# Kernel optimization log

Measured on AMD Instinct MI355X. Metric: run time of the kernel, lower is better.

The kernel has to match this reference:

```python
import jax, jax.numpy as jnp
import numpy as np

N, E, G = 16384, 131072, 32
EPS = 1e-5


def seg_sum(x, ids, n):
    return jax.ops.segment_sum(x, ids, num_segments=n)


def seg_max(x, ids, n):
    return jax.ops.segment_max(x, ids, num_segments=n)


def gcn_conv(x, w, b, src, dst, n):
    # PyG GCNConv: add self loops, symmetric deg normalization
    loop = jnp.arange(n)
    s = jnp.concatenate([src, loop])
    d = jnp.concatenate([dst, loop])
    deg = seg_sum(jnp.ones_like(d, dtype=x.dtype), d, n)
    dis = jax.lax.rsqrt(deg)
    h = x @ w
    norm = (dis[s] * dis[d])[:, None]
    return seg_sum(h[s] * norm, d, n) + b


def sage_conv(x, wl, wr, b, src, dst, n):
    # mean aggregation of source features into target nodes
    cnt = seg_sum(jnp.ones_like(dst, dtype=x.dtype), dst, n)
    agg = seg_sum(x[src], dst, n) / jnp.maximum(cnt, 1.0)[:, None]
    return agg @ wl + x @ wr + b


def gat_conv(x, w, a_src, a_dst, b, src, dst, n, heads=4, ch=256):
    loop = jnp.arange(n)
    s = jnp.concatenate([src, loop])
    d = jnp.concatenate([dst, loop])
    h = (x @ w).reshape(n, heads, ch)            # [N,H,C]
    es = jnp.sum(h * a_src, axis=-1)             # [N,H]
    ed = jnp.sum(h * a_dst, axis=-1)             # [N,H]
    e = jax.nn.leaky_relu(es[s] + ed[d], 0.2)    # [E2,H]
    m = seg_max(e, d, n)
    ex = jnp.exp(e - m[d])
    z = seg_sum(ex, d, n)
    alpha = ex / z[d]                            # softmax over incoming edges
    out = seg_sum(h[s] * alpha[:, :, None], d, n)  # [N,H,C]
    return out.mean(axis=1) + b                  # concat=False -> head mean


def batchnorm(x, g, b):
    mu = x.mean(axis=0)
    var = x.var(axis=0)
    return (x - mu) * jax.lax.rsqrt(var + EPS) * g + b


def setup_inputs() -> dict:
    key = jax.random.key(0)
    ks = jax.random.split(key, 16)
    def w(k, shape, fan_in):
        return jax.random.normal(k, shape, jnp.float32) * (1.0 / np.sqrt(fan_in))
    return {
        "x": jax.random.uniform(ks[0], (N, 5), jnp.float32),
        "edge_index": jax.random.randint(ks[1], (2, E), 0, N),
        "batch": jnp.sort(jax.random.randint(ks[2], (N,), 0, G)),
        "gcn1_w": w(ks[3], (5, 64), 5), "gcn1_b": jnp.zeros((64,), jnp.float32),
        "sage_wl": w(ks[4], (64, 128), 64), "sage_wr": w(ks[5], (64, 128), 64),
        "sage_b": jnp.zeros((128,), jnp.float32),
        "gat_w": w(ks[6], (128, 1024), 128),
        "gat_asrc": w(ks[7], (4, 256), 256), "gat_adst": w(ks[8], (4, 256), 256),
        "gat_b": jnp.zeros((256,), jnp.float32),
        "gcn4_w": w(ks[9], (256, 512), 256), "gcn4_b": jnp.zeros((512,), jnp.float32),
        "bn1_g": jnp.ones((64,), jnp.float32), "bn1_b": jnp.zeros((64,), jnp.float32),
        "bn2_g": jnp.ones((128,), jnp.float32), "bn2_b": jnp.zeros((128,), jnp.float32),
        "bn3_g": jnp.ones((256,), jnp.float32), "bn3_b": jnp.zeros((256,), jnp.float32),
        "bn4_g": jnp.ones((512,), jnp.float32), "bn4_b": jnp.zeros((512,), jnp.float32),
        "fc_w": w(ks[10], (1024, 1024), 1024), "fc_b": jnp.zeros((1024,), jnp.float32),
    }


def reference(x, edge_index, batch, gcn1_w, gcn1_b, sage_wl, sage_wr, sage_b,
              gat_w, gat_asrc, gat_adst, gat_b, gcn4_w, gcn4_b,
              bn1_g, bn1_b, bn2_g, bn2_b, bn3_g, bn3_b, bn4_g, bn4_b,
              fc_w, fc_b):
    src, dst = edge_index[0], edge_index[1]
    n = x.shape[0]
    h = jax.nn.relu(batchnorm(gcn_conv(x, gcn1_w, gcn1_b, src, dst, n), bn1_g, bn1_b))
    h = jax.nn.relu(batchnorm(sage_conv(h, sage_wl, sage_wr, sage_b, src, dst, n), bn2_g, bn2_b))
    h = jax.nn.relu(batchnorm(gat_conv(h, gat_w, gat_asrc, gat_adst, gat_b, src, dst, n), bn3_g, bn3_b))
    h = jax.nn.relu(batchnorm(gcn_conv(h, gcn4_w, gcn4_b, src, dst, n), bn4_g, bn4_b))
    # global mean / max pooling over graphs in the batch
    cnt = seg_sum(jnp.ones((n,), h.dtype), batch, G)
    mean_p = seg_sum(h, batch, G) / jnp.maximum(cnt, 1.0)[:, None]
    max_p = seg_max(h, batch, G)
    max_p = jnp.where(cnt[:, None] > 0, max_p, 0.0)
    pooled = jnp.concatenate([mean_p, max_p], axis=1)  # [G,1024]
    return pooled @ fc_w + fc_b
```

## Files before the change

### kernel.cpp

```cpp
#include <hip/hip_runtime.h>

#define N_ 16384
#define E_ 131072
#define G_ 32
#define EPSF 1e-5f

typedef unsigned short bf16u;
typedef __attribute__((ext_vector_type(8))) short s8v;
typedef __attribute__((ext_vector_type(4))) float f4v;

__device__ __forceinline__ bf16u f2bf(float v) {
    union { float f; unsigned u; } x; x.f = v;
    unsigned r = x.u + 0x7FFF + ((x.u >> 16) & 1);
    return (bf16u)(r >> 16);
}
__device__ __forceinline__ float bf2f(bf16u u) {
    union { unsigned u; float f; } x; x.u = (unsigned)u << 16;
    return x.f;
}

static const size_t OFF_INDEG = 0;
static const size_t OFF_ROWS  = 65536;
static const size_t OFF_CURSOR= 131584;
static const size_t OFF_CSR   = 197120;
static const size_t OFF_DIS   = 721408;
static const size_t OFF_ES    = 786944;
static const size_t OFF_ED    = 1049088;
static const size_t OFF_BNS   = 1311232;
static const size_t OFF_BNQ   = 1376768;
static const size_t OFF_GB    = 1442304;
static const size_t OFF_CNT   = 1442444;
static const size_t OFF_POOL  = 1442560;
static const size_t OFF_MSET  = 1573632;
static const size_t OFF_PART  = 1573632;
static const size_t OFF_BN1C  = 1578752;
static const size_t OFF_XA    = 1786624;
static const size_t OFF_AB    = 5980928;
static const size_t OFF_H2P   = 10175232;
static const size_t OFF_H2B   = 14369536;
static const size_t OFF_H3B   = 18563840;
static const size_t OFF_AGG   = 35328768;
static const size_t OFF_XA4B  = 52105984;
static const size_t OFF_WT1   = 68883200;
static const size_t OFF_WT2   = 69145344;
static const size_t OFF_WT3   = 69407488;
static const size_t OFF_H4B   = 69440256;
static const size_t OFF_VES   = 86479616;
static const size_t OFF_VED   = 86481664;

__global__ __launch_bounds__(1024) void k_scan(const int* __restrict__ indeg,
                                               int* __restrict__ rows,
                                               int* __restrict__ cursor,
                                               float* __restrict__ dis) {
    __shared__ int part[1024];
    int t = threadIdx.x;
    int base = t * 16;
    int local[16];
    int s = 0;
#pragma unroll
    for (int i = 0; i < 16; ++i) {
        local[i] = indeg[base + i]; s += local[i];
        dis[base + i] = rsqrtf((float)local[i] + 1.0f);
    }
    part[t] = s;
    __syncthreads();
    for (int off = 1; off < 1024; off <<= 1) {
        int v = (t >= off) ? part[t - off] : 0;
        __syncthreads();
        part[t] += v;
        __syncthreads();
    }
    int run = (t == 0) ? 0 : part[t - 1];
#pragma unroll
    for (int i = 0; i < 16; ++i) {
        rows[base + i] = run; cursor[base + i] = run; run += local[i];
    }
    if (t == 1023) rows[N_] = run;
}

__global__ void k_fill(const int* __restrict__ src, const int* __restrict__ dst,
                       int* __restrict__ cursor, int* __restrict__ csr) {
    int e = blockIdx.x * 256 + threadIdx.x;
    if (e < E_) {
        int p = atomicAdd(&cursor[dst[e]], 1);
        csr[p] = src[e];
    }
}

__global__ void k_wconv_all(const float* __restrict__ gat_w,
                            const float* __restrict__ gcn4_w,
                            const float* __restrict__ wl, const float* __restrict__ wr,
                            const int* __restrict__ batch,
                            const float* __restrict__ gat_as,
                            const float* __restrict__ gat_ad,
                            const int* __restrict__ dstE,
                            bf16u* __restrict__ wT1, bf16u* __restrict__ wT2,
                            bf16u* __restrict__ wT3, int* __restrict__ gb,
                            float* __restrict__ ves, float* __restrict__ ved,
                            int* __restrict__ indeg) {
    int idx = blockIdx.x * 256 + threadIdx.x;
    if (idx < 131072) {
        int c = idx >> 9;
        int kk = idx & 511;
        int h = kk >> 7, k = kk & 127;
        wT1[idx] = f2bf(0.25f * gat_w[(size_t)k * 1024 + h * 256 + c]);
    } else if (idx < 262144) {
        int j = idx - 131072;
        int m = j >> 8, k = j & 255;
        wT2[j] = f2bf(gcn4_w[(size_t)k * 512 + m]);
    } else if (idx < 278528) {
        int j = idx - 262144;
        int m = j >> 7, k = j & 127;
        float v = (k < 64) ? wl[k*128 + m] : wr[(k-64)*128 + m];
        wT3[j] = f2bf(v);
    } else if (idx < 278592) {
        int g = idx - 278528;
        if (g > G_) return;
        if (g == G_) { gb[G_] = N_; return; }
        int lo = 0, hi = N_;
        while (lo < hi) { int mid = (lo + hi) >> 1; if (batch[mid] < g) lo = mid + 1; else hi = mid; }
        gb[g] = lo;
    } else if (idx < 279104) {
        int j = idx - 278592;
        int h = j >> 7, k = j & 127;
        float s = 0.f;
        for (int c = 0; c < 256; ++c)
            s += gat_w[(size_t)k * 1024 + h*256 + c] * gat_as[h*256 + c];
        ves[j] = s;
    } else if (idx < 279616) {
        int j = idx - 279104;
        int h = j >> 7, k = j & 127;
        float s = 0.f;
        for (int c = 0; c < 256; ++c)
            s += gat_w[(size_t)k * 1024 + h*256 + c] * gat_ad[h*256 + c];
        ved[j] = s;
    } else if (idx < 410688) {
        int e = idx - 279616;
        atomicAdd(&indeg[dstE[e]], 1);
    }
}

__global__ __launch_bounds__(256) void k_gcn1x(const float* __restrict__ x,
                                               const float* __restrict__ dis,
                                               const int* __restrict__ rows,
                                               const int* __restrict__ csr,
                                               float* __restrict__ xa) {
    int wave = threadIdx.x >> 6, lane = threadIdx.x & 63;
    int i = blockIdx.x * 4 + wave;
    float a0=0,a1=0,a2=0,a3=0,a4=0;
    int e0 = rows[i], e1 = rows[i+1];
    for (int e = e0 + lane; e < e1; e += 64) {
        int s = csr[e];
        float wt = dis[s];
        a0 += x[s*5+0]*wt; a1 += x[s*5+1]*wt; a2 += x[s*5+2]*wt;
        a3 += x[s*5+3]*wt; a4 += x[s*5+4]*wt;
    }
#pragma unroll
    for (int off = 32; off > 0; off >>= 1) {
        a0 += __shfl_xor(a0, off, 64); a1 += __shfl_xor(a1, off, 64);
        a2 += __shfl_xor(a2, off, 64); a3 += __shfl_xor(a3, off, 64);
        a4 += __shfl_xor(a4, off, 64);
    }
    float di = dis[i];
    float v0 = di*(a0 + di*x[i*5+0]);
    float v1 = di*(a1 + di*x[i*5+1]);
    float v2 = di*(a2 + di*x[i*5+2]);
    float v3 = di*(a3 + di*x[i*5+3]);
    float v4 = di*(a4 + di*x[i*5+4]);
    if (lane < 5) {
        float v = lane == 0 ? v0 : lane == 1 ? v1 : lane == 2 ? v2 : lane == 3 ? v3 : v4;
        xa[(size_t)i*8 + lane] = v;
    }
}

__global__ __launch_bounds__(256) void k_xstats(const float* __restrict__ xa,
                                                float* __restrict__ partial,
                                                int* __restrict__ cnt,
                                                const float* __restrict__ w,
                                                const float* __restrict__ b,
                                                const float* __restrict__ bng,
                                                const float* __restrict__ bnb,
                                                float* __restrict__ sc,
                                                float* __restrict__ sh) {
    __shared__ float wsum[80];
    __shared__ int lastFlag;
    int t = threadIdx.x;
    int tid = blockIdx.x * 256 + t;
    float v0 = xa[(size_t)tid*8+0], v1 = xa[(size_t)tid*8+1], v2 = xa[(size_t)tid*8+2];
    float v3 = xa[(size_t)tid*8+3], v4 = xa[(size_t)tid*8+4];
    float m[20];
    m[0]=v0; m[1]=v1; m[2]=v2; m[3]=v3; m[4]=v4;
    m[5]=v0*v0;  m[6]=v0*v1;  m[7]=v0*v2;  m[8]=v0*v3;  m[9]=v0*v4;
    m[10]=v1*v1; m[11]=v1*v2; m[12]=v1*v3; m[13]=v1*v4;
    m[14]=v2*v2; m[15]=v2*v3; m[16]=v2*v4;
    m[17]=v3*v3; m[18]=v3*v4;
    m[19]=v4*v4;
#pragma unroll
    for (int off = 32; off > 0; off >>= 1)
#pragma unroll
        for (int j = 0; j < 20; ++j) m[j] += __shfl_xor(m[j], off, 64);
    int wave = t >> 6, lane = t & 63;
    if (lane == 0)
#pragma unroll
        for (int j = 0; j < 20; ++j) wsum[wave*20 + j] = m[j];
    __syncthreads();
    if (t < 20) {
        partial[blockIdx.x * 20 + t] = wsum[t] + wsum[20+t] + wsum[40+t] + wsum[60+t];
        __threadfence();
    }
    __syncthreads();
    if (t == 0) lastFlag = (atomicAdd(cnt, 1) == 63);
    __syncthreads();
    if (!lastFlag || t >= 64) return;
    int l = t;
    const float invN = 1.0f / (float)N_;
    float mm[20];
#pragma unroll
    for (int j = 0; j < 20; ++j) {
        float v = partial[l*20 + j];
#pragma unroll
        for (int off = 32; off > 0; off >>= 1) v += __shfl_xor(v, off, 64);
        mm[j] = v * invN;
    }
    int c = l;
    float wc0 = w[c], wc1 = w[64+c], wc2 = w[128+c], wc3 = w[192+c], wc4 = w[256+c];
    float mu = b[c] + mm[0]*wc0 + mm[1]*wc1 + mm[2]*wc2 + mm[3]*wc3 + mm[4]*wc4;
    float var = 0.f;
    var += (mm[5]  - mm[0]*mm[0]) * wc0*wc0;
    var += (mm[6]  - mm[0]*mm[1]) * wc0*wc1 * 2.f;
    var += (mm[7]  - mm[0]*mm[2]) * wc0*wc2 * 2.f;
    var += (mm[8]  - mm[0]*mm[3]) * wc0*wc3 * 2.f;
    var += (mm[9]  - mm[0]*mm[4]) * wc0*wc4 * 2.f;
    var += (mm[10] - mm[1]*mm[1]) * wc1*wc1;
    var += (mm[11] - mm[1]*mm[2]) * wc1*wc2 * 2.f;
    var += (mm[12] - mm[1]*mm[3]) * wc1*wc3 * 2.f;
    var += (mm[13] - mm[1]*mm[4]) * wc1*wc4 * 2.f;
    var += (mm[14] - mm[2]*mm[2]) * wc2*wc2;
    var += (mm[15] - mm[2]*mm[3]) * wc2*wc3 * 2.f;
    var += (mm[16] - mm[2]*mm[4]) * wc2*wc4 * 2.f;
    var += (mm[17] - mm[3]*mm[3]) * wc3*wc3;
    var += (mm[18] - mm[3]*mm[4]) * wc3*wc4 * 2.f;
    var += (mm[19] - mm[4]*mm[4]) * wc4*wc4;
    float scale = rsqrtf(var + EPSF) * bng[c];
    sc[c] = scale;
    sh[c] = fmaf(b[c], scale, bnb[c] - mu * scale);
}

__global__ __launch_bounds__(256) void k_sage_l1(const float* __restrict__ xa,
                                                 const float* __restrict__ sc,
                                                 const float* __restrict__ sh,
                                                 const float* __restrict__ w,
                                                 const int* __restrict__ rows,
                                                 const int* __restrict__ csr,
                                                 bf16u* __restrict__ ab) {
    int wave = threadIdx.x >> 6, lane = threadIdx.x & 63;
    int i = blockIdx.x * 4 + wave;
    int c = lane;
    float wc0 = w[c], wc1 = w[64+c], wc2 = w[128+c], wc3 = w[192+c], wc4 = w[256+c];
    float scale = sc[c], base = sh[c];
    {
        float4 p = *(const float4*)&xa[(size_t)i*8];
        float p4 = xa[(size_t)i*8 + 4];
        float t = p.x*wc0 + p.y*wc1 + p.z*wc2 + p.w*wc3 + p4*wc4;
        float v = fmaf(t, scale, base); v = v > 0.f ? v : 0.f;
        ab[(size_t)i*128 + 64 + c] = f2bf(v);
    }
    int e0 = rows[i], e1 = rows[i+1];
    float s = 0.f;
    int e = e0;
    for (; e + 3 < e1; e += 4) {
        int s0 = csr[e], s1 = csr[e+1], s2 = csr[e+2], s3 = csr[e+3];
        float4 q0 = *(const float4*)&xa[(size_t)s0*8]; float r0 = xa[(size_t)s0*8+4];
        float4 q1 = *(const float4*)&xa[(size_t)s1*8]; float r1 = xa[(size_t)s1*8+4];
        float4 q2 = *(const float4*)&xa[(size_t)s2*8]; float r2 = xa[(size_t)s2*8+4];
        float4 q3 = *(const float4*)&xa[(size_t)s3*8]; float r3 = xa[(size_t)s3*8+4];
        float t0 = q0.x*wc0 + q0.y*wc1 + q0.z*wc2 + q0.w*wc3 + r0*wc4;
        float t1 = q1.x*wc0 + q1.y*wc1 + q1.z*wc2 + q1.w*wc3 + r1*wc4;
        float t2 = q2.x*wc0 + q2.y*wc1 + q2.z*wc2 + q2.w*wc3 + r2*wc4;
        float t3 = q3.x*wc0 + q3.y*wc1 + q3.z*wc2 + q3.w*wc3 + r3*wc4;
        float v;
        v = fmaf(t0, scale, base); s += v > 0.f ? v : 0.f;
        v = fmaf(t1, scale, base); s += v > 0.f ? v : 0.f;
        v = fmaf(t2, scale, base); s += v > 0.f ? v : 0.f;
        v = fmaf(t3, scale, base); s += v > 0.f ? v : 0.f;
    }
    for (; e < e1; ++e) {
        int sI = csr[e];
        float4 q = *(const float4*)&xa[(size_t)sI*8]; float r = xa[(size_t)sI*8+4];
        float t = q.x*wc0 + q.y*wc1 + q.z*wc2 + q.w*wc3 + r*wc4;
        float v = fmaf(t, scale, base); s += v > 0.f ? v : 0.f;
    }
    ab[(size_t)i*128 + c] = f2bf(s / fmaxf((float)(e1 - e0), 1.0f));
}

__global__ __launch_bounds__(256) void k_gemm_mfma(const bf16u* __restrict__ A,
                                                   const bf16u* __restrict__ BT,
                                                   const float* __restrict__ bias,
                                                   bf16u* __restrict__ C,
                                                   float* __restrict__ sum,
                                                   float* __restrict__ sumsq,
                                                   int K, int M) {
    __shared__ bf16u As[128][40];
    __shared__ bf16u Bs[128][40];
    int tid = threadIdx.x;
    int wave = tid >> 6, lane = tid & 63;
    int wr = (wave >> 1) * 64, wc = (wave & 1) * 64;
    int row0 = blockIdx.y * 128, col0 = blockIdx.x * 128;
    f4v acc[4][4];
#pragma unroll
    for (int i = 0; i < 4; ++i)
#pragma unroll
        for (int j = 0; j < 4; ++j) acc[i][j] = (f4v)0.0f;

    int sr = tid >> 1;
    int sh = (tid & 1) * 16;
    int lr = lane & 15, lq = lane >> 4;

    for (int k0 = 0; k0 < K; k0 += 32) {
        const bf16u* ap = A + (size_t)(row0 + sr) * K + k0 + sh;
        *(uint4*)&As[sr][sh]     = *(const uint4*)ap;
        *(uint4*)&As[sr][sh + 8] = *(const uint4*)(ap + 8);
        const bf16u* bp = BT + (size_t)(col0 + sr) * K + k0 + sh;
        *(uint4*)&Bs[sr][sh]     = *(const uint4*)bp;
        *(uint4*)&Bs[sr][sh + 8] = *(const uint4*)(bp + 8);
        __syncthreads();
        s8v af[4], bfr[4];
#pragma unroll
        for (int i = 0; i < 4; ++i)
            af[i] = *(const s8v*)&As[wr + i*16 + lr][lq*8];
#pragma unroll
        for (int j = 0; j < 4; ++j)
            bfr[j] = *(const s8v*)&Bs[wc + j*16 + lr][lq*8];
#pragma unroll
        for (int i = 0; i < 4; ++i)
#pragma unroll
            for (int j = 0; j < 4; ++j)
                acc[i][j] = __builtin_amdgcn_mfma_f32_16x16x32_bf16(af[i], bfr[j], acc[i][j], 0, 0, 0);
        __syncthreads();
    }

    int slot = (blockIdx.y & 7) << 9;
#pragma unroll
    for (int j = 0; j < 4; ++j) {
        int col = col0 + wc + j*16 + lr;
        float bv = bias ? bias[col] : 0.f;
        float s = 0.f, q = 0.f;
#pragma unroll
        for (int i = 0; i < 4; ++i) {
#pragma unroll
            for (int r = 0; r < 4; ++r) {
                float v = acc[i][j][r] + bv;
                int row = row0 + wr + i*16 + lq*4 + r;
                C[(size_t)row * M + col] = f2bf(v);
                s += v; q += v*v;
            }
        }
        if (sum) {
            s += __shfl_xor(s, 16, 64); q += __shfl_xor(q, 16, 64);
            s += __shfl_xor(s, 32, 64); q += __shfl_xor(q, 32, 64);
            if (lq == 0) { atomicAdd(&sum[slot + col], s); atomicAdd(&sumsq[slot + col], q); }
        }
    }
}

__global__ __launch_bounds__(256) void k_bn_apply2b_attn(
        const bf16u* __restrict__ hp, const float* __restrict__ sum,
        const float* __restrict__ sumsq, const float* __restrict__ g,
        const float* __restrict__ b, const float* __restrict__ ves,
        const float* __restrict__ ved, bf16u* __restrict__ hb,
        float* __restrict__ es, float* __restrict__ ed) {
    int wave = threadIdx.x >> 6, lane = threadIdx.x & 63;
    int i = blockIdx.x * 4 + wave;
    int c = lane * 2;
    const float invN = 1.0f / (float)N_;
    float sx=0.f, sy=0.f, qx=0.f, qy=0.f;
#pragma unroll
    for (int s8 = 0; s8 < 8; ++s8) {
        float2 a = *(const float2*)&sum[s8*512 + c];
        float2 d = *(const float2*)&sumsq[s8*512 + c];
        sx += a.x; sy += a.y; qx += d.x; qy += d.y;
    }
    float2 gg = *(const float2*)&g[c];
    float2 bb = *(const float2*)&b[c];
    float mu0 = sx*invN, mu1 = sy*invN;
    float sc0 = rsqrtf(qx*invN - mu0*mu0 + EPSF)*gg.x, sh0 = bb.x - mu0*sc0;
    float sc1 = rsqrtf(qy*invN - mu1*mu1 + EPSF)*gg.y, sh1 = bb.y - mu1*sc1;
    unsigned pv = *(const unsigned*)&hp[(size_t)i*128 + c];
    float v0 = bf2f((bf16u)(pv & 0xFFFF));
    float v1 = bf2f((bf16u)(pv >> 16));
    v0 = fmaf(v0, sc0, sh0); v0 = v0 > 0.f ? v0 : 0.f;
    v1 = fmaf(v1, sc1, sh1); v1 = v1 > 0.f ? v1 : 0.f;
    unsigned ow = (unsigned)f2bf(v0) | ((unsigned)f2bf(v1) << 16);
    *(unsigned*)&hb[(size_t)i*128 + c] = ow;
    float vs[4], vd[4];
#pragma unroll
    for (int h = 0; h < 4; ++h) {
        float2 a = *(const float2*)&ves[h*128 + c];
        float2 d = *(const float2*)&ved[h*128 + c];
        vs[h] = v0*a.x + v1*a.y;
        vd[h] = v0*d.x + v1*d.y;
    }
#pragma unroll
    for (int off = 32; off > 0; off >>= 1) {
#pragma unroll
        for (int h = 0; h < 4; ++h) {
            vs[h] += __shfl_xor(vs[h], off, 64);
            vd[h] += __shfl_xor(vd[h], off, 64);
        }
    }
    if (lane == 0) {
        *(float4*)&es[i*4] = make_float4(vs[0], vs[1], vs[2], vs[3]);
        *(float4*)&ed[i*4] = make_float4(vd[0], vd[1], vd[2], vd[3]);
    }
}

__global__ __launch_bounds__(256) void k_gat_agg2(const bf16u* __restrict__ h2b,
                                                  const float* __restrict__ es,
                                                  const float* __restrict__ ed,
                                                  const int* __restrict__ rows,
                                                  const int* __restrict__ csr,
                                                  bf16u* __restrict__ agg) {
    int wave = threadIdx.x >> 6, lane = threadIdx.x & 63;
    int i = blockIdx.x * 4 + wave;
    int c = lane * 2;
    float4 edv = *(const float4*)&ed[i*4];
    float4 sv  = *(const float4*)&es[i*4];
    int e0 = rows[i], e1 = rows[i+1];
    float e, m0, m1, m2, m3;
    e = sv.x + edv.x; m0 = e >= 0.f ? e : 0.2f*e;
    e = sv.y + edv.y; m1 = e >= 0.f ? e : 0.2f*e;
    e = sv.z + edv.z; m2 = e >= 0.f ? e : 0.2f*e;
    e = sv.w + edv.w; m3 = e >= 0.f ? e : 0.2f*e;
    for (int ee = e0 + lane; ee < e1; ee += 64) {
        int s = csr[ee];
        float4 s2 = *(const float4*)&es[s*4];
        e = s2.x + edv.x; m0 = fmaxf(m0, e >= 0.f ? e : 0.2f*e);
        e = s2.y + edv.y; m1 = fmaxf(m1, e >= 0.f ? e : 0.2f*e);
        e = s2.z + edv.z; m2 = fmaxf(m2, e >= 0.f ? e : 0.2f*e);
        e = s2.w + edv.w; m3 = fmaxf(m3, e >= 0.f ? e : 0.2f*e);
    }
#pragma unroll
    for (int off = 32; off > 0; off >>= 1) {
        m0 = fmaxf(m0, __shfl_xor(m0, off, 64));
        m1 = fmaxf(m1, __shfl_xor(m1, off, 64));
        m2 = fmaxf(m2, __shfl_xor(m2, off, 64));
        m3 = fmaxf(m3, __shfl_xor(m3, off, 64));
    }
    float z0, z1, z2, z3;
    float a00, a01, a10, a11, a20, a21, a30, a31;
    {
        e = sv.x + edv.x; e = e >= 0.f ? e : 0.2f*e; z0 = __expf(e - m0);
        e = sv.y + edv.y; e = e >= 0.f ? e : 0.2f*e; z1 = __expf(e - m1);
        e = sv.z + edv.z; e = e >= 0.f ? e : 0.2f*e; z2 = __expf(e - m2);
        e = sv.w + edv.w; e = e >= 0.f ? e : 0.2f*e; z3 = __expf(e - m3);
        unsigned pv = *(const unsigned*)&h2b[(size_t)i*128 + c];
        float v0 = bf2f((bf16u)(pv & 0xFFFF)), v1 = bf2f((bf16u)(pv >> 16));
        a00 = z0*v0; a01 = z0*v1; a10 = z1*v0; a11 = z1*v1;
        a20 = z2*v0; a21 = z2*v1; a30 = z3*v0; a31 = z3*v1;
    }
    int ee = e0;
    for (; ee + 3 < e1; ee += 4) {
        int s0 = csr[ee], s1 = csr[ee+1], s2i = csr[ee+2], s3i = csr[ee+3];
        float4 q0 = *(const float4*)&es[s0*4];
        float4 q1 = *(const float4*)&es[s1*4];
        float4 q2 = *(const float4*)&es[s2i*4];
        float4 q3 = *(const float4*)&es[s3i*4];
        unsigned p0 = *(const unsigned*)&h2b[(size_t)s0*128 + c];
        unsigned p1 = *(const unsigned*)&h2b[(size_t)s1*128 + c];
        unsigned p2 = *(const unsigned*)&h2b[(size_t)s2i*128 + c];
        unsigned p3 = *(const unsigned*)&h2b[(size_t)s3i*128 + c];
        float v0, v1, ex;
        v0 = bf2f((bf16u)(p0 & 0xFFFF)); v1 = bf2f((bf16u)(p0 >> 16));
        e = q0.x + edv.x; e = e >= 0.f ? e : 0.2f*e; ex = __expf(e - m0);
        z0 += ex; a00 = fmaf(ex, v0, a00); a01 = fmaf(ex, v1, a01);
        e = q0.y + edv.y; e = e >= 0.f ? e : 0.2f*e; ex = __expf(e - m1);
        z1 += ex; a10 = fmaf(ex, v0, a10); a11 = fmaf(ex, v1, a11);
        e = q0.z + edv.z; e = e >= 0.f ? e : 0.2f*e; ex = __expf(e - m2);
        z2 += ex; a20 = fmaf(ex, v0, a20); a21 = fmaf(ex, v1, a21);
        e = q0.w + edv.w; e = e >= 0.f ? e : 0.2f*e; ex = __expf(e - m3);
        z3 += ex; a30 = fmaf(ex, v0, a30); a31 = fmaf(ex, v1, a31);
        v0 = bf2f((bf16u)(p1 & 0xFFFF)); v1 = bf2f((bf16u)(p1 >> 16));
        e = q1.x + edv.x; e = e >= 0.f ? e : 0.2f*e; ex = __expf(e - m0);
        z0 += ex; a00 = fmaf(ex, v0, a00); a01 = fmaf(ex, v1, a01);
        e = q1.y + edv.y; e = e >= 0.f ? e : 0.2f*e; ex = __expf(e - m1);
        z1 += ex; a10 = fmaf(ex, v0, a10); a11 = fmaf(ex, v1, a11);
        e = q1.z + edv.z; e = e >= 0.f ? e : 0.2f*e; ex = __expf(e - m2);
        z2 += ex; a20 = fmaf(ex, v0, a20); a21 = fmaf(ex, v1, a21);
        e = q1.w + edv.w; e = e >= 0.f ? e : 0.2f*e; ex = __expf(e - m3);
        z3 += ex; a30 = fmaf(ex, v0, a30); a31 = fmaf(ex, v1, a31);
        v0 = bf2f((bf16u)(p2 & 0xFFFF)); v1 = bf2f((bf16u)(p2 >> 16));
        e = q2.x + edv.x; e = e >= 0.f ? e : 0.2f*e; ex = __expf(e - m0);
        z0 += ex; a00 = fmaf(ex, v0, a00); a01 = fmaf(ex, v1, a01);
        e = q2.y + edv.y; e = e >= 0.f ? e : 0.2f*e; ex = __expf(e - m1);
        z1 += ex; a10 = fmaf(ex, v0, a10); a11 = fmaf(ex, v1, a11);
        e = q2.z + edv.z; e = e >= 0.f ? e : 0.2f*e; ex = __expf(e - m2);
        z2 += ex; a20 = fmaf(ex, v0, a20); a21 = fmaf(ex, v1, a21);
        e = q2.w + edv.w; e = e >= 0.f ? e : 0.2f*e; ex = __expf(e - m3);
        z3 += ex; a30 = fmaf(ex, v0, a30); a31 = fmaf(ex, v1, a31);
        v0 = bf2f((bf16u)(p3 & 0xFFFF)); v1 = bf2f((bf16u)(p3 >> 16));
        e = q3.x + edv.x; e = e >= 0.f ? e : 0.2f*e; ex = __expf(e - m0);
        z0 += ex; a00 = fmaf(ex, v0, a00); a01 = fmaf(ex, v1, a01);
        e = q3.y + edv.y; e = e >= 0.f ? e : 0.2f*e; ex = __expf(e - m1);
        z1 += ex; a10 = fmaf(ex, v0, a10); a11 = fmaf(ex, v1, a11);
        e = q3.z + edv.z; e = e >= 0.f ? e : 0.2f*e; ex = __expf(e - m2);
        z2 += ex; a20 = fmaf(ex, v0, a20); a21 = fmaf(ex, v1, a21);
        e = q3.w + edv.w; e = e >= 0.f ? e : 0.2f*e; ex = __expf(e - m3);
        z3 += ex; a30 = fmaf(ex, v0, a30); a31 = fmaf(ex, v1, a31);
    }
    for (; ee < e1; ++ee) {
        int s = csr[ee];
        float4 s2 = *(const float4*)&es[s*4];
        unsigned pv = *(const unsigned*)&h2b[(size_t)s*128 + c];
        float v0 = bf2f((bf16u)(pv & 0xFFFF)), v1 = bf2f((bf16u)(pv >> 16));
        float ex;
        e = s2.x + edv.x; e = e >= 0.f ? e : 0.2f*e; ex = __expf(e - m0);
        z0 += ex; a00 = fmaf(ex, v0, a00); a01 = fmaf(ex, v1, a01);
        e = s2.y + edv.y; e = e >= 0.f ? e : 0.2f*e; ex = __expf(e - m1);
        z1 += ex; a10 = fmaf(ex, v0, a10); a11 = fmaf(ex, v1, a11);
        e = s2.z + edv.z; e = e >= 0.f ? e : 0.2f*e; ex = __expf(e - m2);
        z2 += ex; a20 = fmaf(ex, v0, a20); a21 = fmaf(ex, v1, a21);
        e = s2.w + edv.w; e = e >= 0.f ? e : 0.2f*e; ex = __expf(e - m3);
        z3 += ex; a30 = fmaf(ex, v0, a30); a31 = fmaf(ex, v1, a31);
    }
    size_t base = (size_t)i * 512 + c;
    float r; unsigned ow;
    r = 1.f/z0; ow = (unsigned)f2bf(a00*r) | ((unsigned)f2bf(a01*r) << 16);
    *(unsigned*)&agg[base]       = ow;
    r = 1.f/z1; ow = (unsigned)f2bf(a10*r) | ((unsigned)f2bf(a11*r) << 16);
    *(unsigned*)&agg[base + 128] = ow;
    r = 1.f/z2; ow = (unsigned)f2bf(a20*r) | ((unsigned)f2bf(a21*r) << 16);
    *(unsigned*)&agg[base + 256] = ow;
    r = 1.f/z3; ow = (unsigned)f2bf(a30*r) | ((unsigned)f2bf(a31*r) << 16);
    *(unsigned*)&agg[base + 384] = ow;
}

__global__ __launch_bounds__(256) void k_gcn4_agg(const bf16u* __restrict__ h3b,
                                                  const float* __restrict__ dis,
                                                  const int* __restrict__ rows,
                                                  const int* __restrict__ csr,
                                                  const float* __restrict__ sum,
                                                  const float* __restrict__ sumsq,
                                                  const float* __restrict__ g,
                                                  const float* __restrict__ b,
                                                  bf16u* __restrict__ xab) {
    int wave = threadIdx.x >> 6, q = threadIdx.x & 63;
    int i = blockIdx.x * 4 + wave;
    int c = q * 4;
    const float invN = 1.0f / (float)N_;
    float4 sm = make_float4(0.f,0.f,0.f,0.f), sq = make_float4(0.f,0.f,0.f,0.f);
#pragma unroll
    for (int s8 = 0; s8 < 8; ++s8) {
        float4 a = *(const float4*)&sum[s8*512 + c];
        float4 d = *(const float4*)&sumsq[s8*512 + c];
        sm.x += a.x; sm.y += a.y; sm.z += a.z; sm.w += a.w;
        sq.x += d.x; sq.y += d.y; sq.z += d.z; sq.w += d.w;
    }
    float4 gg = *(const float4*)&g[c];
    float4 bb = *(const float4*)&b[c];
    float mu, sc0, sc1, sc2, sc3, sh0, sh1, sh2, sh3;
    mu = sm.x*invN; sc0 = rsqrtf(sq.x*invN - mu*mu + EPSF)*gg.x; sh0 = bb.x - mu*sc0;
    mu = sm.y*invN; sc1 = rsqrtf(sq.y*invN - mu*mu + EPSF)*gg.y; sh1 = bb.y - mu*sc1;
    mu = sm.z*invN; sc2 = rsqrtf(sq.z*invN - mu*mu + EPSF)*gg.z; sh2 = bb.z - mu*sc2;
    mu = sm.w*invN; sc3 = rsqrtf(sq.w*invN - mu*mu + EPSF)*gg.w; sh3 = bb.w - mu*sc3;
    float di = dis[i];
    float a0, a1, a2, a3;
    {
        ushort4 u = *(const ushort4*)(h3b + (size_t)i*256 + c);
        float v, dd = di * di;
        v = fmaf(bf2f(u.x), sc0, sh0); v = v > 0.f ? v : 0.f; a0 = v * dd;
        v = fmaf(bf2f(u.y), sc1, sh1); v = v > 0.f ? v : 0.f; a1 = v * dd;
        v = fmaf(bf2f(u.z), sc2, sh2); v = v > 0.f ? v : 0.f; a2 = v * dd;
        v = fmaf(bf2f(u.w), sc3, sh3); v = v > 0.f ? v : 0.f; a3 = v * dd;
    }
    int e0 = rows[i], e1 = rows[i+1];
    int e = e0;
    for (; e + 3 < e1; e += 4) {
        int s0 = csr[e], s1 = csr[e+1], s2i = csr[e+2], s3i = csr[e+3];
        float w0 = dis[s0] * di, w1 = dis[s1] * di, w2 = dis[s2i] * di, w3 = dis[s3i] * di;
        ushort4 u0 = *(const ushort4*)(h3b + (size_t)s0*256 + c);
        ushort4 u1 = *(const ushort4*)(h3b + (size_t)s1*256 + c);
        ushort4 u2 = *(const ushort4*)(h3b + (size_t)s2i*256 + c);
        ushort4 u3 = *(const ushort4*)(h3b + (size_t)s3i*256 + c);
        float v;
        v = fmaf(bf2f(u0.x), sc0, sh0); v = v > 0.f ? v : 0.f; a0 += v * w0;
        v = fmaf(bf2f(u0.y), sc1, sh1); v = v > 0.f ? v : 0.f; a1 += v * w0;
        v = fmaf(bf2f(u0.z), sc2, sh2); v = v > 0.f ? v : 0.f; a2 += v * w0;
        v = fmaf(bf2f(u0.w), sc3, sh3); v = v > 0.f ? v : 0.f; a3 += v * w0;
        v = fmaf(bf2f(u1.x), sc0, sh0); v = v > 0.f ? v : 0.f; a0 += v * w1;
        v = fmaf(bf2f(u1.y), sc1, sh1); v = v > 0.f ? v : 0.f; a1 += v * w1;
        v = fmaf(bf2f(u1.z), sc2, sh2); v = v > 0.f ? v : 0.f; a2 += v * w1;
        v = fmaf(bf2f(u1.w), sc3, sh3); v = v > 0.f ? v : 0.f; a3 += v * w1;
        v = fmaf(bf2f(u2.x), sc0, sh0); v = v > 0.f ? v : 0.f; a0 += v * w2;
        v = fmaf(bf2f(u2.y), sc1, sh1); v = v > 0.f ? v : 0.f; a1 += v * w2;
        v = fmaf(bf2f(u2.z), sc2, sh2); v = v > 0.f ? v : 0.f; a2 += v * w2;
        v = fmaf(bf2f(u2.w), sc3, sh3); v = v > 0.f ? v : 0.f; a3 += v * w2;
        v = fmaf(bf2f(u3.x), sc0, sh0); v = v > 0.f ? v : 0.f; a0 += v * w3;
        v = fmaf(bf2f(u3.y), sc1, sh1); v = v > 0.f ? v : 0.f; a1 += v * w3;
        v = fmaf(bf2f(u3.z), sc2, sh2); v = v > 0.f ? v : 0.f; a2 += v * w3;
        v = fmaf(bf2f(u3.w), sc3, sh3); v = v > 0.f ? v : 0.f; a3 += v * w3;
    }
    for (; e < e1; ++e) {
        int s = csr[e];
        float w = dis[s] * di;
        ushort4 u = *(const ushort4*)(h3b + (size_t)s*256 + c);
        float v;
        v = fmaf(bf2f(u.x), sc0, sh0); v = v > 0.f ? v : 0.f; a0 += v * w;
        v = fmaf(bf2f(u.y), sc1, sh1); v = v > 0.f ? v : 0.f; a1 += v * w;
        v = fmaf(bf2f(u.z), sc2, sh2); v = v > 0.f ? v : 0.f; a2 += v * w;
        v = fmaf(bf2f(u.w), sc3, sh3); v = v > 0.f ? v : 0.f; a3 += v * w;
    }
    ushort4 o;
    o.x = f2bf(a0); o.y = f2bf(a1); o.z = f2bf(a2); o.w = f2bf(a3);
    *(ushort4*)(xab + (size_t)i*256 + c) = o;
}

__global__ void k_pool(const bf16u* __restrict__ h4b, const int* __restrict__ gb,
                       const float* __restrict__ sum, const float* __restrict__ sumsq,
                       const float* __restrict__ g, const float* __restrict__ b,
                       const float* __restrict__ fcb,
                       float* __restrict__ pooled, float* __restrict__ out) {
    int bidx = blockIdx.x;
    int t = threadIdx.x;
    if (bidx >= 512) {
        int i = (bidx - 512) * 256 + t;
        out[i] = fcb[i & 1023];
        return;
    }
    int gi = bidx >> 4;
    int chunk = bidx & 15;
    const float invN = 1.0f / (float)N_;
    float su0=0.f, qq0=0.f, su1=0.f, qq1=0.f;
#pragma unroll
    for (int s8 = 0; s8 < 8; ++s8) {
        su0 += sum[s8*512 + t];       qq0 += sumsq[s8*512 + t];
        su1 += sum[s8*512 + 256 + t]; qq1 += sumsq[s8*512 + 256 + t];
    }
    float mu0 = su0 * invN;
    float sc0 = rsqrtf(qq0 * invN - mu0*mu0 + EPSF) * g[t];
    float sh0 = b[t] - mu0 * sc0;
    float mu1 = su1 * invN;
    float sc1 = rsqrtf(qq1 * invN - mu1*mu1 + EPSF) * g[t+256];
    float sh1 = b[t+256] - mu1 * sc1;
    int r0g = gb[gi], r1g = gb[gi+1];
    int n = r1g - r0g;
    if (n <= 0) return;
    int per = (n + 15) >> 4;
    int r0 = r0g + chunk * per;
    int r1 = min(r0 + per, r1g);
    if (r0 >= r1) return;
    float s0=0.f, s1=0.f, m0=0.f, m1=0.f;
    for (int r = r0; r < r1; ++r) {
        float v = fmaf(bf2f(h4b[(size_t)r*512 + t]), sc0, sh0);
        v = v > 0.f ? v : 0.f;
        s0 += v; m0 = fmaxf(m0, v);
        float w = fmaf(bf2f(h4b[(size_t)r*512 + 256 + t]), sc1, sh1);
        w = w > 0.f ? w : 0.f;
        s1 += w; m1 = fmaxf(m1, w);
    }
    atomicAdd(&pooled[gi*1024 + t], s0);
    atomicAdd(&pooled[gi*1024 + 256 + t], s1);
    atomicMax((int*)&pooled[gi*1024 + 512 + t],  __float_as_int(m0));
    atomicMax((int*)&pooled[gi*1024 + 768 + t],  __float_as_int(m1));
}

#define FCKZ 16
#define FCKC (1024 / FCKZ)

__global__ __launch_bounds__(256) void k_fc2(const float* __restrict__ pooled,
                                             const float* __restrict__ w,
                                             const int* __restrict__ gb,
                                             float* __restrict__ out) {
    __shared__ float pr[FCKC];
    int g = blockIdx.x;
    int z = blockIdx.y;
    int t = threadIdx.x;
    int k0 = z * FCKC;
    if (t < FCKC) {
        float scale = (z < 8) ? 1.0f / fmaxf((float)(gb[g+1] - gb[g]), 1.0f) : 1.0f;
        pr[t] = pooled[g * 1024 + k0 + t] * scale;
    }
    __syncthreads();
    int m0 = t * 4;
    float ax = 0.f, ay = 0.f, az = 0.f, aw = 0.f;
#pragma unroll 8
    for (int k = 0; k < FCKC; ++k) {
        const float4 wv = *(const float4*)&w[(size_t)(k0 + k) * 1024 + m0];
        float p = pr[k];
        ax += p * wv.x; ay += p * wv.y; az += p * wv.z; aw += p * wv.w;
    }
    atomicAdd(&out[g * 1024 + m0 + 0], ax);
    atomicAdd(&out[g * 1024 + m0 + 1], ay);
    atomicAdd(&out[g * 1024 + m0 + 2], az);
    atomicAdd(&out[g * 1024 + m0 + 3], aw);
}

extern "C" void kernel_launch(void* const* d_in, const int* in_sizes, int n_in,
                              void* d_out, int out_size, void* d_ws, size_t ws_size,
                              hipStream_t stream) {
    (void)in_sizes; (void)n_in; (void)out_size; (void)ws_size;
    const float* x       = (const float*)d_in[0];
    const int*   ei      = (const int*)d_in[1];
    const int*   batch   = (const int*)d_in[2];
    const float* gcn1_w  = (const float*)d_in[3];
    const float* gcn1_b  = (const float*)d_in[4];
    const float* sage_wl = (const float*)d_in[5];
    const float* sage_wr = (const float*)d_in[6];
    const float* sage_b  = (const float*)d_in[7];
    const float* gat_w   = (const float*)d_in[8];
    const float* gat_as  = (const float*)d_in[9];
    const float* gat_ad  = (const float*)d_in[10];
    const float* gat_b   = (const float*)d_in[11];
    const float* gcn4_w  = (const float*)d_in[12];
    const float* gcn4_b  = (const float*)d_in[13];
    const float* bn1_g   = (const float*)d_in[14];
    const float* bn1_b   = (const float*)d_in[15];
    const float* bn2_g   = (const float*)d_in[16];
    const float* bn2_b   = (const float*)d_in[17];
    const float* bn3_g   = (const float*)d_in[18];
    const float* bn3_b   = (const float*)d_in[19];
    const float* bn4_g   = (const float*)d_in[20];
    const float* bn4_b   = (const float*)d_in[21];
    const float* fc_w    = (const float*)d_in[22];
    const float* fc_b    = (const float*)d_in[23];
    float* out = (float*)d_out;

    char* w8 = (char*)d_ws;
    int*   indeg  = (int*)(w8 + OFF_INDEG);
    int*   rows   = (int*)(w8 + OFF_ROWS);
    int*   cursor = (int*)(w8 + OFF_CURSOR);
    int*   csr    = (int*)(w8 + OFF_CSR);
    float* dis    = (float*)(w8 + OFF_DIS);
    float* es     = (float*)(w8 + OFF_ES);
    float* ed     = (float*)(w8 + OFF_ED);
    float* bns    = (float*)(w8 + OFF_BNS);
    float* bnq    = (float*)(w8 + OFF_BNQ);
    int*   gb     = (int*)(w8 + OFF_GB);
    int*   cnt    = (int*)(w8 + OFF_CNT);
    float* pooled = (float*)(w8 + OFF_POOL);
    float* part   = (float*)(w8 + OFF_PART);
    float* bn1sc  = (float*)(w8 + OFF_BN1C);
    float* bn1sh  = (float*)(w8 + OFF_BN1C + 256);
    float* xa     = (float*)(w8 + OFF_XA);
    bf16u* ab     = (bf16u*)(w8 + OFF_AB);
    bf16u* h2p    = (bf16u*)(w8 + OFF_H2P);
    bf16u* h2b    = (bf16u*)(w8 + OFF_H2B);
    bf16u* h3b    = (bf16u*)(w8 + OFF_H3B);
    bf16u* agg    = (bf16u*)(w8 + OFF_AGG);
    bf16u* xa4b   = (bf16u*)(w8 + OFF_XA4B);
    bf16u* wT1    = (bf16u*)(w8 + OFF_WT1);
    bf16u* wT2    = (bf16u*)(w8 + OFF_WT2);
    bf16u* wT3    = (bf16u*)(w8 + OFF_WT3);
    bf16u* h4b    = (bf16u*)(w8 + OFF_H4B);
    float* ves    = (float*)(w8 + OFF_VES);
    float* ved    = (float*)(w8 + OFF_VED);

    const int* srcE = ei;
    const int* dstE = ei + E_;

    hipMemsetAsync(w8, 0, OFF_MSET, stream);
    k_wconv_all<<<1605, 256, 0, stream>>>(gat_w, gcn4_w, sage_wl, sage_wr, batch,
                                          gat_as, gat_ad, dstE,
                                          wT1, wT2, wT3, gb, ves, ved, indeg);
    k_scan<<<1, 1024, 0, stream>>>(indeg, rows, cursor, dis);
    k_fill<<<E_/256, 256, 0, stream>>>(srcE, dstE, cursor, csr);

    k_gcn1x<<<N_/4, 256, 0, stream>>>(x, dis, rows, csr, xa);
    k_xstats<<<64, 256, 0, stream>>>(xa, part, cnt, gcn1_w, gcn1_b, bn1_g, bn1_b,
                                     bn1sc, bn1sh);
    k_sage_l1<<<N_/4, 256, 0, stream>>>(xa, bn1sc, bn1sh, gcn1_w, rows, csr, ab);

    {
        dim3 grid(1, N_/128);
        k_gemm_mfma<<<grid, 256, 0, stream>>>(ab, wT3, sage_b, h2p,
                                              bns + 4096, bnq + 4096, 128, 128);
    }
    k_bn_apply2b_attn<<<N_/4, 256, 0, stream>>>(h2p, bns + 4096, bnq + 4096, bn2_g, bn2_b,
                                                ves, ved, h2b, es, ed);

    k_gat_agg2<<<N_/4, 256, 0, stream>>>(h2b, es, ed, rows, csr, agg);
    {
        dim3 grid(256/128, N_/128);
        k_gemm_mfma<<<grid, 256, 0, stream>>>(agg, wT1, gat_b, h3b,
                                              bns + 8192, bnq + 8192, 512, 256);
    }

    k_gcn4_agg<<<N_/4, 256, 0, stream>>>(h3b, dis, rows, csr, bns + 8192, bnq + 8192,
                                         bn3_g, bn3_b, xa4b);
    {
        dim3 grid(512/128, N_/128);
        k_gemm_mfma<<<grid, 256, 0, stream>>>(xa4b, wT2, gcn4_b, h4b,
                                              bns + 12288, bnq + 12288, 256, 512);
    }

    k_pool<<<640, 256, 0, stream>>>(h4b, gb, bns + 12288, bnq + 12288, bn4_g, bn4_b,
                                    fc_b, pooled, out);

    {
        dim3 grid(G_, FCKZ);
        k_fc2<<<grid, 256, 0, stream>>>(pooled, fc_w, gb, out);
    }
}
```

Measured before the change: 287.8 us.

## Drop GAT max pass, use wave-shuffle scan, coalesce weight transposes, regroup workspace

The GAT aggregation kernel no longer does a separate pass over incoming edges to find the softmax max. It uses the self-loop logit as the reference and clamps each exponent at 80 to avoid overflow. The CSR scan replaces the 1024-step shared-memory Hillis-Steele loop with wave-level shuffle scans, and the weight-transpose kernel now reads inputs coalesced and scatters the writes. Workspace offsets are reordered so the memset-cleared buffers sit together. The clamp changes numerics when an edge logit exceeds the self-loop logit by more than 80, which may hurt accuracy.

```diff
diff --git a/kernel.cpp b/kernel.cpp
--- a/kernel.cpp
+++ b/kernel.cpp
@@ -20,20 +20,20 @@
 }
 
 static const size_t OFF_INDEG = 0;
-static const size_t OFF_ROWS  = 65536;
-static const size_t OFF_CURSOR= 131584;
-static const size_t OFF_CSR   = 197120;
-static const size_t OFF_DIS   = 721408;
-static const size_t OFF_ES    = 786944;
-static const size_t OFF_ED    = 1049088;
-static const size_t OFF_BNS   = 1311232;
-static const size_t OFF_BNQ   = 1376768;
-static const size_t OFF_GB    = 1442304;
-static const size_t OFF_CNT   = 1442444;
-static const size_t OFF_POOL  = 1442560;
-static const size_t OFF_MSET  = 1573632;
-static const size_t OFF_PART  = 1573632;
-static const size_t OFF_BN1C  = 1578752;
+static const size_t OFF_BNS   = 65536;
+static const size_t OFF_BNQ   = 131072;
+static const size_t OFF_POOL  = 196608;
+static const size_t OFF_GB    = 327680;
+static const size_t OFF_CNT   = 327816;
+static const size_t OFF_MSET  = 327936;
+static const size_t OFF_ROWS  = 327936;
+static const size_t OFF_CURSOR= 393728;
+static const size_t OFF_CSR   = 459264;
+static const size_t OFF_DIS   = 983552;
+static const size_t OFF_ES    = 1049088;
+static const size_t OFF_ED    = 1311232;
+static const size_t OFF_PART  = 1573376;
+static const size_t OFF_BN1C  = 1578496;
 static const size_t OFF_XA    = 1786624;
 static const size_t OFF_AB    = 5980928;
 static const size_t OFF_H2P   = 10175232;
@@ -52,8 +52,9 @@
                                                int* __restrict__ rows,
                                                int* __restrict__ cursor,
                                                float* __restrict__ dis) {
-    __shared__ int part[1024];
+    __shared__ int wtot[16];
     int t = threadIdx.x;
+    int lane = t & 63, wave = t >> 6;
     int base = t * 16;
     int local[16];
     int s = 0;
@@ -62,15 +63,25 @@
         local[i] = indeg[base + i]; s += local[i];
         dis[base + i] = rsqrtf((float)local[i] + 1.0f);
     }
-    part[t] = s;
+    int own = s;
+#pragma unroll
+    for (int off = 1; off < 64; off <<= 1) {
+        int v = __shfl_up(s, off, 64);
+        if (lane >= off) s += v;
+    }
+    if (lane == 63) wtot[wave] = s;
     __syncthreads();
-    for (int off = 1; off < 1024; off <<= 1) {
-        int v = (t >= off) ? part[t - off] : 0;
-        __syncthreads();
-        part[t] += v;
-        __syncthreads();
-    }
-    int run = (t == 0) ? 0 : part[t - 1];
+    if (wave == 0) {
+        int v = (lane < 16) ? wtot[lane] : 0;
+#pragma unroll
+        for (int off = 1; off < 16; off <<= 1) {
+            int u = __shfl_up(v, off, 64);
+            if (lane >= off) v += u;
+        }
+        if (lane < 16) wtot[lane] = v;
+    }
+    __syncthreads();
+    int run = s - own + (wave > 0 ? wtot[wave - 1] : 0);
 #pragma unroll
     for (int i = 0; i < 16; ++i) {
         rows[base + i] = run; cursor[base + i] = run; run += local[i];
@@ -100,19 +111,21 @@
                             int* __restrict__ indeg) {
     int idx = blockIdx.x * 256 + threadIdx.x;
     if (idx < 131072) {
-        int c = idx >> 9;
-        int kk = idx & 511;
-        int h = kk >> 7, k = kk & 127;
-        wT1[idx] = f2bf(0.25f * gat_w[(size_t)k * 1024 + h * 256 + c]);
+        int k = idx >> 10, col = idx & 1023;
+        int h = col >> 8, c = col & 255;
+        wT1[(size_t)c * 512 + h * 128 + k] = f2bf(0.25f * gat_w[idx]);
     } else if (idx < 262144) {
         int j = idx - 131072;
-        int m = j >> 8, k = j & 255;
-        wT2[j] = f2bf(gcn4_w[(size_t)k * 512 + m]);
+        int k = j >> 9, m = j & 511;
+        wT2[m * 256 + k] = f2bf(gcn4_w[j]);
+    } else if (idx < 270336) {
+        int j = idx - 262144;
+        int k = j >> 7, m = j & 127;
+        wT3[m * 128 + k] = f2bf(wl[j]);
     } else if (idx < 278528) {
-        int j = idx - 262144;
-        int m = j >> 7, k = j & 127;
-        float v = (k < 64) ? wl[k*128 + m] : wr[(k-64)*128 + m];
-        wT3[j] = f2bf(v);
+        int j = idx - 270336;
+        int k = j >> 7, m = j & 127;
+        wT3[m * 128 + 64 + k] = f2bf(wr[j]);
     } else if (idx < 278592) {
         int g = idx - 278528;
         if (g > G_) return;
@@ -431,33 +444,16 @@
     e = sv.y + edv.y; m1 = e >= 0.f ? e : 0.2f*e;
     e = sv.z + edv.z; m2 = e >= 0.f ? e : 0.2f*e;
     e = sv.w + edv.w; m3 = e >= 0.f ? e : 0.2f*e;
-    for (int ee = e0 + lane; ee < e1; ee += 64) {
-        int s = csr[ee];
-        float4 s2 = *(const float4*)&es[s*4];
-        e = s2.x + edv.x; m0 = fmaxf(m0, e >= 0.f ? e : 0.2f*e);
-        e = s2.y + edv.y; m1 = fmaxf(m1, e >= 0.f ? e : 0.2f*e);
-        e = s2.z + edv.z; m2 = fmaxf(m2, e >= 0.f ? e : 0.2f*e);
-        e = s2.w + edv.w; m3 = fmaxf(m3, e >= 0.f ? e : 0.2f*e);
-    }
-#pragma unroll
-    for (int off = 32; off > 0; off >>= 1) {
-        m0 = fmaxf(m0, __shfl_xor(m0, off, 64));
-        m1 = fmaxf(m1, __shfl_xor(m1, off, 64));
-        m2 = fmaxf(m2, __shfl_xor(m2, off, 64));
-        m3 = fmaxf(m3, __shfl_xor(m3, off, 64));
-    }
     float z0, z1, z2, z3;
     float a00, a01, a10, a11, a20, a21, a30, a31;
     {
-        e = sv.x + edv.x; e = e >= 0.f ? e : 0.2f*e; z0 = __expf(e - m0);
-        e = sv.y + edv.y; e = e >= 0.f ? e : 0.2f*e; z1 = __expf(e - m1);
-        e = sv.z + edv.z; e = e >= 0.f ? e : 0.2f*e; z2 = __expf(e - m2);
-        e = sv.w + edv.w; e = e >= 0.f ? e : 0.2f*e; z3 = __expf(e - m3);
+        z0 = 1.f; z1 = 1.f; z2 = 1.f; z3 = 1.f;
         unsigned pv = *(const unsigned*)&h2b[(size_t)i*128 + c];
         float v0 = bf2f((bf16u)(pv & 0xFFFF)), v1 = bf2f((bf16u)(pv >> 16));
-        a00 = z0*v0; a01 = z0*v1; a10 = z1*v0; a11 = z1*v1;
-        a20 = z2*v0; a21 = z2*v1; a30 = z3*v0; a31 = z3*v1;
-    }
+        a00 = v0; a01 = v1; a10 = v0; a11 = v1;
+        a20 = v0; a21 = v1; a30 = v0; a31 = v1;
+    }
+#define GEXP(Q, EDC, M) __expf(fminf(((Q) + (EDC) >= 0.f ? (Q) + (EDC) : 0.2f*((Q) + (EDC))) - (M), 80.f))
     int ee = e0;
     for (; ee + 3 < e1; ee += 4) {
         int s0 = csr[ee], s1 = csr[ee+1], s2i = csr[ee+2], s3i = csr[ee+3];
@@ -471,41 +467,25 @@
         unsigned p3 = *(const unsigned*)&h2b[(size_t)s3i*128 + c];
         float v0, v1, ex;
         v0 = bf2f((bf16u)(p0 & 0xFFFF)); v1 = bf2f((bf16u)(p0 >> 16));
-        e = q0.x + edv.x; e = e >= 0.f ? e : 0.2f*e; ex = __expf(e - m0);
-        z0 += ex; a00 = fmaf(ex, v0, a00); a01 = fmaf(ex, v1, a01);
-        e = q0.y + edv.y; e = e >= 0.f ? e : 0.2f*e; ex = __expf(e - m1);
-        z1 += ex; a10 = fmaf(ex, v0, a10); a11 = fmaf(ex, v1, a11);
-        e = q0.z + edv.z; e = e >= 0.f ? e : 0.2f*e; ex = __expf(e - m2);
-        z2 += ex; a20 = fmaf(ex, v0, a20); a21 = fmaf(ex, v1, a21);
-        e = q0.w + edv.w; e = e >= 0.f ? e : 0.2f*e; ex = __expf(e - m3);
-        z3 += ex; a30 = fmaf(ex, v0, a30); a31 = fmaf(ex, v1, a31);
+        ex = GEXP(q0.x, edv.x, m0); z0 += ex; a00 = fmaf(ex, v0, a00); a01 = fmaf(ex, v1, a01);
+        ex = GEXP(q0.y, edv.y, m1); z1 += ex; a10 = fmaf(ex, v0, a10); a11 = fmaf(ex, v1, a11);
+        ex = GEXP(q0.z, edv.z, m2); z2 += ex; a20 = fmaf(ex, v0, a20); a21 = fmaf(ex, v1, a21);
+        ex = GEXP(q0.w, edv.w, m3); z3 += ex; a30 = fmaf(ex, v0, a30); a31 = fmaf(ex, v1, a31);
         v0 = bf2f((bf16u)(p1 & 0xFFFF)); v1 = bf2f((bf16u)(p1 >> 16));
-        e = q1.x + edv.x; e = e >= 0.f ? e : 0.2f*e; ex = __expf(e - m0);
-        z0 += ex; a00 = fmaf(ex, v0, a00); a01 = fmaf(ex, v1, a01);
-        e = q1.y + edv.y; e = e >= 0.f ? e : 0.2f*e; ex = __expf(e - m1);
-        z1 += ex; a10 = fmaf(ex, v0, a10); a11 = fmaf(ex, v1, a11);
-        e = q1.z + edv.z; e = e >= 0.f ? e : 0.2f*e; ex = __expf(e - m2);
-        z2 += ex; a20 = fmaf(ex, v0, a20); a21 = fmaf(ex, v1, a21);
-        e = q1.w + edv.w; e = e >= 0.f ? e : 0.2f*e; ex = __expf(e - m3);
-        z3 += ex; a30 = fmaf(ex, v0, a30); a31 = fmaf(ex, v1, a31);
+        ex = GEXP(q1.x, edv.x, m0); z0 += ex; a00 = fmaf(ex, v0, a00); a01 = fmaf(ex, v1, a01);
+        ex = GEXP(q1.y, edv.y, m1); z1 += ex; a10 = fmaf(ex, v0, a10); a11 = fmaf(ex, v1, a11);
+        ex = GEXP(q1.z, edv.z, m2); z2 += ex; a20 = fmaf(ex, v0, a20); a21 = fmaf(ex, v1, a21);
+        ex = GEXP(q1.w, edv.w, m3); z3 += ex; a30 = fmaf(ex, v0, a30); a31 = fmaf(ex, v1, a31);
         v0 = bf2f((bf16u)(p2 & 0xFFFF)); v1 = bf2f((bf16u)(p2 >> 16));
-        e = q2.x + edv.x; e = e >= 0.f ? e : 0.2f*e; ex = __expf(e - m0);
-        z0 += ex; a00 = fmaf(ex, v0, a00); a01 = fmaf(ex, v1, a01);
-        e = q2.y + edv.y; e = e >= 0.f ? e : 0.2f*e; ex = __expf(e - m1);
-        z1 += ex; a10 = fmaf(ex, v0, a10); a11 = fmaf(ex, v1, a11);
-        e = q2.z + edv.z; e = e >= 0.f ? e : 0.2f*e; ex = __expf(e - m2);
-        z2 += ex; a20 = fmaf(ex, v0, a20); a21 = fmaf(ex, v1, a21);
-        e = q2.w + edv.w; e = e >= 0.f ? e : 0.2f*e; ex = __expf(e - m3);
-        z3 += ex; a30 = fmaf(ex, v0, a30); a31 = fmaf(ex, v1, a31);
+        ex = GEXP(q2.x, edv.x, m0); z0 += ex; a00 = fmaf(ex, v0, a00); a01 = fmaf(ex, v1, a01);
+        ex = GEXP(q2.y, edv.y, m1); z1 += ex; a10 = fmaf(ex, v0, a10); a11 = fmaf(ex, v1, a11);
+        ex = GEXP(q2.z, edv.z, m2); z2 += ex; a20 = fmaf(ex, v0, a20); a21 = fmaf(ex, v1, a21);
+        ex = GEXP(q2.w, edv.w, m3); z3 += ex; a30 = fmaf(ex, v0, a30); a31 = fmaf(ex, v1, a31);
         v0 = bf2f((bf16u)(p3 & 0xFFFF)); v1 = bf2f((bf16u)(p3 >> 16));
-        e = q3.x + edv.x; e = e >= 0.f ? e : 0.2f*e; ex = __expf(e - m0);
-        z0 += ex; a00 = fmaf(ex, v0, a00); a01 = fmaf(ex, v1, a01);
-        e = q3.y + edv.y; e = e >= 0.f ? e : 0.2f*e; ex = __expf(e - m1);
-        z1 += ex; a10 = fmaf(ex, v0, a10); a11 = fmaf(ex, v1, a11);
-        e = q3.z + edv.z; e = e >= 0.f ? e : 0.2f*e; ex = __expf(e - m2);
-        z2 += ex; a20 = fmaf(ex, v0, a20); a21 = fmaf(ex, v1, a21);
-        e = q3.w + edv.w; e = e >= 0.f ? e : 0.2f*e; ex = __expf(e - m3);
-        z3 += ex; a30 = fmaf(ex, v0, a30); a31 = fmaf(ex, v1, a31);
+        ex = GEXP(q3.x, edv.x, m0); z0 += ex; a00 = fmaf(ex, v0, a00); a01 = fmaf(ex, v1, a01);
+        ex = GEXP(q3.y, edv.y, m1); z1 += ex; a10 = fmaf(ex, v0, a10); a11 = fmaf(ex, v1, a11);
+        ex = GEXP(q3.z, edv.z, m2); z2 += ex; a20 = fmaf(ex, v0, a20); a21 = fmaf(ex, v1, a21);
+        ex = GEXP(q3.w, edv.w, m3); z3 += ex; a30 = fmaf(ex, v0, a30); a31 = fmaf(ex, v1, a31);
     }
     for (; ee < e1; ++ee) {
         int s = csr[ee];
@@ -513,15 +493,12 @@
         unsigned pv = *(const unsigned*)&h2b[(size_t)s*128 + c];
         float v0 = bf2f((bf16u)(pv & 0xFFFF)), v1 = bf2f((bf16u)(pv >> 16));
         float ex;
-        e = s2.x + edv.x; e = e >= 0.f ? e : 0.2f*e; ex = __expf(e - m0);
-        z0 += ex; a00 = fmaf(ex, v0, a00); a01 = fmaf(ex, v1, a01);
-        e = s2.y + edv.y; e = e >= 0.f ? e : 0.2f*e; ex = __expf(e - m1);
-        z1 += ex; a10 = fmaf(ex, v0, a10); a11 = fmaf(ex, v1, a11);
-        e = s2.z + edv.z; e = e >= 0.f ? e : 0.2f*e; ex = __expf(e - m2);
-        z2 += ex; a20 = fmaf(ex, v0, a20); a21 = fmaf(ex, v1, a21);
-        e = s2.w + edv.w; e = e >= 0.f ? e : 0.2f*e; ex = __expf(e - m3);
-        z3 += ex; a30 = fmaf(ex, v0, a30); a31 = fmaf(ex, v1, a31);
-    }
+        ex = GEXP(s2.x, edv.x, m0); z0 += ex; a00 = fmaf(ex, v0, a00); a01 = fmaf(ex, v1, a01);
+        ex = GEXP(s2.y, edv.y, m1); z1 += ex; a10 = fmaf(ex, v0, a10); a11 = fmaf(ex, v1, a11);
+        ex = GEXP(s2.z, edv.z, m2); z2 += ex; a20 = fmaf(ex, v0, a20); a21 = fmaf(ex, v1, a21);
+        ex = GEXP(s2.w, edv.w, m3); z3 += ex; a30 = fmaf(ex, v0, a30); a31 = fmaf(ex, v1, a31);
+    }
+#undef GEXP
     size_t base = (size_t)i * 512 + c;
     float r; unsigned ow;
     r = 1.f/z0; ow = (unsigned)f2bf(a00*r) | ((unsigned)f2bf(a01*r) << 16);
@@ -726,17 +703,17 @@
 
     char* w8 = (char*)d_ws;
     int*   indeg  = (int*)(w8 + OFF_INDEG);
+    float* bns    = (float*)(w8 + OFF_BNS);
+    float* bnq    = (float*)(w8 + OFF_BNQ);
+    float* pooled = (float*)(w8 + OFF_POOL);
+    int*   gb     = (int*)(w8 + OFF_GB);
+    int*   cnt    = (int*)(w8 + OFF_CNT);
     int*   rows   = (int*)(w8 + OFF_ROWS);
     int*   cursor = (int*)(w8 + OFF_CURSOR);
     int*   csr    = (int*)(w8 + OFF_CSR);
     float* dis    = (float*)(w8 + OFF_DIS);
     float* es     = (float*)(w8 + OFF_ES);
     float* ed     = (float*)(w8 + OFF_ED);
-    float* bns    = (float*)(w8 + OFF_BNS);
-    float* bnq    = (float*)(w8 + OFF_BNQ);
-    int*   gb     = (int*)(w8 + OFF_GB);
-    int*   cnt    = (int*)(w8 + OFF_CNT);
-    float* pooled = (float*)(w8 + OFF_POOL);
     float* part   = (float*)(w8 + OFF_PART);
     float* bn1sc  = (float*)(w8 + OFF_BN1C);
     float* bn1sh  = (float*)(w8 + OFF_BN1C + 256);
```

After: 285.5 us, median of 2. No clear change (-0.8%).
